# Kernel optimization log

Hardware: AMD Instinct MI355X
Metric: run time of the kernel (lower is better)

The kernel has to match this reference:

```python
import jax, jax.numpy as jnp
import numpy as np


def _bilinear_resample(inputs, offsets):
    # inputs: (b, s, s, c); offsets: (b, s, s, 2) -- faithful to tf_batch_map_offsets
    b, h, w, c = inputs.shape
    s = h  # square map assumed by original code (input_size = shape[1])
    n = h * w
    offs = offsets.reshape(b, n, 2)
    gi, gj = jnp.meshgrid(jnp.arange(s, dtype=inputs.dtype),
                          jnp.arange(s, dtype=inputs.dtype), indexing='ij')
    grid = jnp.stack([gi, gj], axis=-1).reshape(1, n, 2)
    coords = jnp.clip(offs + grid, 0.0, float(s - 1))  # (b, n, 2), [i, j]
    lt = jnp.floor(coords).astype(jnp.int32)  # (b, n, 2)
    rb = jnp.ceil(coords).astype(jnp.int32)
    bidx = jnp.arange(b)[:, None]  # (b, 1) broadcasts with (b, n) index maps

    def gather(ci, cj):
        return inputs[bidx, ci, cj]  # (b, n, c)

    vals_lt = gather(lt[..., 0], lt[..., 1])
    vals_rb = gather(rb[..., 0], rb[..., 1])
    vals_lb = gather(rb[..., 0], lt[..., 1])  # [ceil_i, floor_j]
    vals_rt = gather(lt[..., 0], rb[..., 1])  # [floor_i, ceil_j]

    frac = coords - lt.astype(coords.dtype)  # (b, n, 2) fractional offsets
    fy = frac[..., 1:2]  # column fraction (axis 1 of coords)
    fx = frac[..., 0:1]  # row fraction
    vals_t = vals_lt + (vals_rt - vals_lt) * fy
    vals_b = vals_lb + (vals_rb - vals_lb) * fy
    out = vals_t + (vals_b - vals_t) * fx  # (b, n, c)
    return out.reshape(b, h, w, c)


def setup_inputs() -> dict:
    key = jax.random.key(0)
    k1, k2 = jax.random.split(key)
    B, S, C = 16, 128, 128
    offsets = jax.random.normal(k1, (B, S, S, 2), dtype=jnp.float32)
    inputs = jax.random.normal(k2, (B, S, S, C), dtype=jnp.float32)
    return {"offsets": offsets, "inputs": inputs}


def reference(offsets, inputs):
    return _bilinear_resample(inputs, offsets)
```

## Files before the change

### kernel.cpp

```cpp
#include <hip/hip_runtime.h>


constexpr int S = 128;
constexpr int CVEC = 32;
constexpr int PIX_PER_BLOCK = 16;

typedef float f32x4 __attribute__((ext_vector_type(4)));

__device__ __forceinline__ void tap_setup(int pix, int lane_c, float2 off,
                                          int& i00, int& i01, int& i10, int& i11,
                                          float& fy, float& fx)
{
    const int j   = pix & (S - 1);
    const int rem = pix >> 7;
    const int i   = rem & (S - 1);
    const int b   = rem >> 7;

    float y = fminf(fmaxf((float)i + off.x, 0.0f), (float)(S - 1));
    float x = fminf(fmaxf((float)j + off.y, 0.0f), (float)(S - 1));

    const float y0f = floorf(y);
    const float x0f = floorf(x);
    const int y0 = (int)y0f;
    const int x0 = (int)x0f;
    const int y1 = min(y0 + 1, S - 1);
    const int x1 = min(x0 + 1, S - 1);
    fy = y - y0f;
    fx = x - x0f;

    const int base = (b * S * S) * CVEC + lane_c;
    const int r0 = base + y0 * (S * CVEC);
    const int r1 = base + y1 * (S * CVEC);
    i00 = r0 + x0 * CVEC;
    i01 = r0 + x1 * CVEC;
    i10 = r1 + x0 * CVEC;
    i11 = r1 + x1 * CVEC;
}

__global__ __launch_bounds__(256) void resample_kernel(
    const float2* __restrict__ offsets2,
    const f32x4*  __restrict__ inputs4,
    f32x4*        __restrict__ out4)
{
    const int tid    = threadIdx.x;
    const int lane_c = tid & 31;
    const int pg     = tid >> 5;
    const int pix0   = blockIdx.x * PIX_PER_BLOCK + pg;
    const int pix1   = pix0 + 8;

    const float2 off0 = offsets2[pix0];
    const float2 off1 = offsets2[pix1];

    int a00, a01, a10, a11; float fy0, fx0;
    int b00, b01, b10, b11; float fy1, fx1;
    tap_setup(pix0, lane_c, off0, a00, a01, a10, a11, fy0, fx0);
    tap_setup(pix1, lane_c, off1, b00, b01, b10, b11, fy1, fx1);

    f32x4 va00 = __builtin_nontemporal_load(&inputs4[a00]);
    f32x4 va01 = __builtin_nontemporal_load(&inputs4[a01]);
    f32x4 va10 = __builtin_nontemporal_load(&inputs4[a10]);
    f32x4 va11 = __builtin_nontemporal_load(&inputs4[a11]);
    f32x4 vb00 = __builtin_nontemporal_load(&inputs4[b00]);
    f32x4 vb01 = __builtin_nontemporal_load(&inputs4[b01]);
    f32x4 vb10 = __builtin_nontemporal_load(&inputs4[b10]);
    f32x4 vb11 = __builtin_nontemporal_load(&inputs4[b11]);
    asm volatile("" : "+v"(va00), "+v"(va01), "+v"(va10), "+v"(va11),
                      "+v"(vb00), "+v"(vb01), "+v"(vb10), "+v"(vb11));

    const f32x4 vt0 = va00 + (va01 - va00) * fx0;
    const f32x4 vb0 = va10 + (va11 - va10) * fx0;
    const f32x4 o0  = vt0 + (vb0 - vt0) * fy0;
    const f32x4 vt1 = vb00 + (vb01 - vb00) * fx1;
    const f32x4 vb1 = vb10 + (vb11 - vb10) * fx1;
    const f32x4 o1  = vt1 + (vb1 - vt1) * fy1;

    __builtin_nontemporal_store(o0, &out4[(long long)pix0 * CVEC + lane_c]);
    __builtin_nontemporal_store(o1, &out4[(long long)pix1 * CVEC + lane_c]);
}

extern "C" void kernel_launch(void* const* d_in, const int* in_sizes, int n_in,
                              void* d_out, int out_size, void* d_ws, size_t ws_size,
                              hipStream_t stream) {
    const float2* offsets2 = (const float2*)d_in[0];
    const f32x4*  inputs4  = (const f32x4*)d_in[1];
    f32x4*        out4     = (f32x4*)d_out;

    const int B = in_sizes[0] / (S * S * 2);
    const int total_pix = B * S * S;
    const int blocks = total_pix / PIX_PER_BLOCK;

    resample_kernel<<<blocks, 256, 0, stream>>>(offsets2, inputs4, out4);
}
```

Measured before the change: 241.7 us.

## Loop over eight pixels per warp-group with software-pipelined gather prefetch

Each block now handles 64 pixels instead of 16. Each 32-lane group loops eight times, prefetching the next pixel's four taps and offsets while it interpolates and stores the current one. The input loads also switch from nontemporal to regular cached loads, so neighbouring taps that are reused can hit in cache. The aim is fewer blocks, less launch and setup overhead, and hidden gather latency. In exchange there is less parallelism per block, a serial dependency across iterations, and more register pressure.

```diff
diff --git a/kernel.cpp b/kernel.cpp
--- a/kernel.cpp
+++ b/kernel.cpp
@@ -3,7 +3,8 @@
 
 constexpr int S = 128;
 constexpr int CVEC = 32;
-constexpr int PIX_PER_BLOCK = 16;
+constexpr int ITERS = 8;
+constexpr int PIX_PER_BLOCK = 8 * ITERS;
 
 typedef float f32x4 __attribute__((ext_vector_type(4)));
 
@@ -45,37 +46,49 @@
     const int tid    = threadIdx.x;
     const int lane_c = tid & 31;
     const int pg     = tid >> 5;
-    const int pix0   = blockIdx.x * PIX_PER_BLOCK + pg;
-    const int pix1   = pix0 + 8;
+    const int p0     = blockIdx.x * PIX_PER_BLOCK + pg;
 
-    const float2 off0 = offsets2[pix0];
-    const float2 off1 = offsets2[pix1];
+    float2 offA = offsets2[p0];
+    float2 offB = offsets2[p0 + 8];
 
-    int a00, a01, a10, a11; float fy0, fx0;
-    int b00, b01, b10, b11; float fy1, fx1;
-    tap_setup(pix0, lane_c, off0, a00, a01, a10, a11, fy0, fx0);
-    tap_setup(pix1, lane_c, off1, b00, b01, b10, b11, fy1, fx1);
+    int a00, a01, a10, a11; float fyA, fxA;
+    tap_setup(p0, lane_c, offA, a00, a01, a10, a11, fyA, fxA);
+    f32x4 v00 = inputs4[a00];
+    f32x4 v01 = inputs4[a01];
+    f32x4 v10 = inputs4[a10];
+    f32x4 v11 = inputs4[a11];
 
-    f32x4 va00 = __builtin_nontemporal_load(&inputs4[a00]);
-    f32x4 va01 = __builtin_nontemporal_load(&inputs4[a01]);
-    f32x4 va10 = __builtin_nontemporal_load(&inputs4[a10]);
-    f32x4 va11 = __builtin_nontemporal_load(&inputs4[a11]);
-    f32x4 vb00 = __builtin_nontemporal_load(&inputs4[b00]);
-    f32x4 vb01 = __builtin_nontemporal_load(&inputs4[b01]);
-    f32x4 vb10 = __builtin_nontemporal_load(&inputs4[b10]);
-    f32x4 vb11 = __builtin_nontemporal_load(&inputs4[b11]);
-    asm volatile("" : "+v"(va00), "+v"(va01), "+v"(va10), "+v"(va11),
-                      "+v"(vb00), "+v"(vb01), "+v"(vb10), "+v"(vb11));
+    #pragma unroll
+    for (int it = 0; it < ITERS; ++it) {
+        const int pix = p0 + it * 8;
 
-    const f32x4 vt0 = va00 + (va01 - va00) * fx0;
-    const f32x4 vb0 = va10 + (va11 - va10) * fx0;
-    const f32x4 o0  = vt0 + (vb0 - vt0) * fy0;
-    const f32x4 vt1 = vb00 + (vb01 - vb00) * fx1;
-    const f32x4 vb1 = vb10 + (vb11 - vb10) * fx1;
-    const f32x4 o1  = vt1 + (vb1 - vt1) * fy1;
+        float2 offC = offB;
+        if (it + 2 < ITERS) offC = offsets2[p0 + (it + 2) * 8];
 
-    __builtin_nontemporal_store(o0, &out4[(long long)pix0 * CVEC + lane_c]);
-    __builtin_nontemporal_store(o1, &out4[(long long)pix1 * CVEC + lane_c]);
+        f32x4 w00, w01, w10, w11;
+        float fyB = 0.f, fxB = 0.f;
+        if (it + 1 < ITERS) {
+            int b00, b01, b10, b11;
+            tap_setup(p0 + (it + 1) * 8, lane_c, offB,
+                      b00, b01, b10, b11, fyB, fxB);
+            w00 = inputs4[b00];
+            w01 = inputs4[b01];
+            w10 = inputs4[b10];
+            w11 = inputs4[b11];
+            asm volatile("" : "+v"(w00), "+v"(w01), "+v"(w10), "+v"(w11));
+        }
+
+        const f32x4 vt = v00 + (v01 - v00) * fxA;
+        const f32x4 vb = v10 + (v11 - v10) * fxA;
+        const f32x4 o  = vt + (vb - vt) * fyA;
+        __builtin_nontemporal_store(o, &out4[(long long)pix * CVEC + lane_c]);
+
+        if (it + 1 < ITERS) {
+            v00 = w00; v01 = w01; v10 = w10; v11 = w11;
+            fyA = fyB; fxA = fxB;
+            offB = offC;
+        }
+    }
 }
 
 extern "C" void kernel_launch(void* const* d_in, const int* in_sizes, int n_in,
```

After: 236.9 us. 1.02x faster.
